# Kernel optimization log

Measured on AMD Instinct MI355X. Metric: run time of the kernel, lower is better.

Reference implementation:

```python
import jax, jax.numpy as jnp
import numpy as np

N, L, H, D = 2, 4096, 12, 64
HD = H * D

def setup_inputs() -> dict:
    key = jax.random.key(0)
    ks = jax.random.split(key, 5)
    s = 1.0 / np.sqrt(HD)  # keep projections well-scaled
    return {
        "x": jax.random.normal(ks[0], (N, L, HD), dtype=jnp.float32),
        "Wq": jax.random.normal(ks[1], (HD, HD), dtype=jnp.float32) * s,
        "bq": jnp.zeros((HD,), dtype=jnp.float32),
        "Wk": jax.random.normal(ks[2], (HD, HD), dtype=jnp.float32) * s,
        "bk": jnp.zeros((HD,), dtype=jnp.float32),
        "Wv": jax.random.normal(ks[3], (HD, HD), dtype=jnp.float32) * s,
        "bv": jnp.zeros((HD,), dtype=jnp.float32),
        "Wo": jax.random.normal(ks[4], (HD, HD), dtype=jnp.float32) * s,
        "bo": jnp.zeros((HD,), dtype=jnp.float32),
        "train": 0,
    }

def reference(x, Wq, bq, Wk, bk, Wv, bv, Wo, bo, train):
    n, l, hd = x.shape
    h, d = H, D
    # QKV projections (hk.Linear: x @ W + b), reshape to (n, l, h, d)
    q = (x @ Wq + bq).reshape(n, l, h, d)
    k = (x @ Wk + bk).reshape(n, l, h, d)
    v = (x @ Wv + bv).reshape(n, l, h, d)
    # scores: (n, q, k, h), scaled by sqrt(key_size)
    qkt = jnp.einsum('nqhd,nkhd->nqkh', q, k) / jnp.sqrt(jnp.float32(d))
    attn = jax.nn.softmax(qkt, axis=2)
    # eval mode: dropout_rate is 0.0, so dropout is identity
    o = jnp.einsum('nqkh,nkhd->nqhd', attn, v).reshape(n, l, hd)
    return o @ Wo + bo
```

## Files before the change

kernel.cpp:

```cpp
#include <hip/hip_runtime.h>

#define NN 2
#define LL 4096
#define HH 12
#define DD 64
#define HD_ 768
#define M_TOT (NN * LL)
#define KVSTRIDE 262144

typedef __bf16 bf16_t;
typedef _Float16 f16_t;
typedef __bf16 bf16x8 __attribute__((ext_vector_type(8)));
typedef __bf16 bf16x4 __attribute__((ext_vector_type(4)));
typedef _Float16 f16x2 __attribute__((ext_vector_type(2)));
typedef _Float16 f16x4 __attribute__((ext_vector_type(4)));
typedef _Float16 f16x8 __attribute__((ext_vector_type(8)));
typedef float floatx4 __attribute__((ext_vector_type(4)));
typedef float floatx16 __attribute__((ext_vector_type(16)));

#define QSCALE 0.1803368801111f

__device__ __forceinline__ void async_load16(const void* g, void* l) {
    __builtin_amdgcn_global_load_lds(
        (const __attribute__((address_space(1))) unsigned int*)(g),
        (__attribute__((address_space(3))) unsigned int*)(l),
        16, 0, 0);
}

__device__ __forceinline__ f16x2 pkrtz(float a, float b) {
    return __builtin_bit_cast(f16x2, __builtin_amdgcn_cvt_pkrtz(a, b));
}

__device__ __forceinline__ f16x4 shflx32(f16x4 v) {
    int2 iv = __builtin_bit_cast(int2, v);
    iv.x = __shfl_xor(iv.x, 32);
    iv.y = __shfl_xor(iv.y, 32);
    return __builtin_bit_cast(f16x4, iv);
}

__global__ void cvt_kernel(const float* __restrict__ src, bf16_t* __restrict__ dst, int n4) {
    int i = blockIdx.x * blockDim.x + threadIdx.x;
    if (i < n4) {
        const float4 v = ((const float4*)src)[i];
        bf16_t* d = dst + (size_t)i * 4;
        d[0] = (bf16_t)v.x; d[1] = (bf16_t)v.y; d[2] = (bf16_t)v.z; d[3] = (bf16_t)v.w;
    }
}

struct WtArgs { const float* W[4]; bf16_t* Wt[4]; };
__global__ void cvt_wt_kernel(WtArgs a) {
    const int z = blockIdx.z;
    int id = blockIdx.x * 256 + threadIdx.x;
    int k = id / HD_;
    int n = id % HD_;
    a.Wt[z][(size_t)n * HD_ + k] = (bf16_t)a.W[z][id];
}

__device__ __forceinline__ void gemm_tile64(
    const bf16_t* __restrict__ A, const bf16_t* __restrict__ Bt,
    bf16_t* As, bf16_t* Bs, int m0, int n0, floatx4 (&acc)[2][2])
{
    const int tid  = threadIdx.x;
    const int lane = tid & 63;
    const int quad = lane >> 4, l16 = lane & 15;
    const int wave = tid >> 6;
    const int wm = wave >> 1, wn = wave & 1;
    const int lrow = tid >> 2;
    const int lcol = (tid & 3) * 16;

    for (int kt = 0; kt < HD_; kt += 64) {
        __syncthreads();
        {
            const bf16_t* ga = A + (size_t)(m0 + lrow) * HD_ + kt + lcol;
            *(bf16x8*)&As[lrow * 72 + lcol]     = *(const bf16x8*)ga;
            *(bf16x8*)&As[lrow * 72 + lcol + 8] = *(const bf16x8*)(ga + 8);
            const bf16_t* gb = Bt + (size_t)(n0 + lrow) * HD_ + kt + lcol;
            *(bf16x8*)&Bs[lrow * 72 + lcol]     = *(const bf16x8*)gb;
            *(bf16x8*)&Bs[lrow * 72 + lcol + 8] = *(const bf16x8*)(gb + 8);
        }
        __syncthreads();
        for (int ks = 0; ks < 2; ++ks) {
            bf16x8 af[2], bfr[2];
            af[0]  = *(const bf16x8*)&As[(wm * 32 + l16) * 72 + ks * 32 + quad * 8];
            af[1]  = *(const bf16x8*)&As[(wm * 32 + 16 + l16) * 72 + ks * 32 + quad * 8];
            bfr[0] = *(const bf16x8*)&Bs[(wn * 32 + l16) * 72 + ks * 32 + quad * 8];
            bfr[1] = *(const bf16x8*)&Bs[(wn * 32 + 16 + l16) * 72 + ks * 32 + quad * 8];
            for (int mi = 0; mi < 2; ++mi)
                for (int ni = 0; ni < 2; ++ni)
                    acc[mi][ni] = __builtin_amdgcn_mfma_f32_16x16x32_bf16(
                        af[mi], bfr[ni], acc[mi][ni], 0, 0, 0);
        }
    }
}

struct QKVArgs {
    const bf16_t* Bt[3];
    const float* bias[3];
    void* out[3];
};
__global__ __launch_bounds__(256) void gemm_qkv_kernel(const bf16_t* __restrict__ A, QKVArgs p)
{
    __shared__ __align__(16) bf16_t As[64 * 72];
    __shared__ __align__(16) bf16_t Bs[64 * 72];
    const int z = blockIdx.z;
    const int m0 = blockIdx.y * 64, n0 = blockIdx.x * 64;

    floatx4 acc[2][2] = {};
    gemm_tile64(A, p.Bt[z], As, Bs, m0, n0, acc);

    const int tid  = threadIdx.x;
    const int lane = tid & 63;
    const int quad = lane >> 4, l16 = lane & 15;
    const int wave = tid >> 6;
    const int wm = wave >> 1, wn = wave & 1;
    const float scale = (z == 0) ? QSCALE : 1.0f;
    const float* bias = p.bias[z];

    for (int ni = 0; ni < 2; ++ni) {
        const int col = n0 + wn * 32 + ni * 16 + l16;
        const float bv = bias[col];
        const int h = col >> 6, d = col & 63;
        for (int mi = 0; mi < 2; ++mi) {
            for (int r = 0; r < 4; ++r) {
                const int row = m0 + wm * 32 + mi * 16 + quad * 4 + r;
                const float val = (acc[mi][ni][r] + bv) * scale;
                const int nn = row >> 12, l = row & 4095;
                const size_t nhb = (size_t)(nn * HH + h) * KVSTRIDE;
                if (z == 0) {
                    ((bf16_t*)p.out[0])[(((size_t)nn * HH + h) * LL + l) * DD + d] = (bf16_t)val;
                } else if (z == 1) {
                    size_t idx = nhb + (size_t)((l >> 5) * 4 + (d >> 4)) * 512
                               + ((l & 31) + 32 * ((d >> 3) & 1)) * 8 + (d & 7);
                    ((bf16_t*)p.out[1])[idx] = (bf16_t)val;
                } else {
                    size_t idx = nhb + (size_t)(((l >> 6) * 2 + (d >> 5)) * 4 + ((l >> 4) & 3)) * 512
                               + ((d & 31) + 32 * ((l >> 3) & 1)) * 8 + (l & 7);
                    ((f16_t*)p.out[2])[idx] = (f16_t)val;
                }
            }
        }
    }
}

__global__ __launch_bounds__(256) void gemm_o_kernel(
    const bf16_t* __restrict__ A, const bf16_t* __restrict__ Bt,
    const float* __restrict__ bias, float* __restrict__ Cout)
{
    __shared__ __align__(16) bf16_t As[64 * 72];
    __shared__ __align__(16) bf16_t Bs[64 * 72];
    const int m0 = blockIdx.y * 64, n0 = blockIdx.x * 64;

    floatx4 acc[2][2] = {};
    gemm_tile64(A, Bt, As, Bs, m0, n0, acc);

    const int tid  = threadIdx.x;
    const int lane = tid & 63;
    const int quad = lane >> 4, l16 = lane & 15;
    const int wave = tid >> 6;
    const int wm = wave >> 1, wn = wave & 1;

    for (int ni = 0; ni < 2; ++ni) {
        const int col = n0 + wn * 32 + ni * 16 + l16;
        const float bv = bias[col];
        for (int mi = 0; mi < 2; ++mi)
            for (int r = 0; r < 4; ++r) {
                const int row = m0 + wm * 32 + mi * 16 + quad * 4 + r;
                Cout[(size_t)row * HD_ + col] = acc[mi][ni][r] + bv;
            }
    }
}

__global__ __launch_bounds__(256) void attn_kernel(
    const bf16_t* __restrict__ qg, const bf16_t* __restrict__ kf,
    const f16_t* __restrict__ vf, bf16_t* __restrict__ og)
{
    __shared__ union {
        struct {
            bf16_t Ks[8 * 512];
            f16_t  Vs[8 * 512];
        } s;
        bf16_t OT[128 * 72];
    } u;

    const int tid = threadIdx.x;
    const int w = tid >> 6, lane = tid & 63;
    const int l32 = lane & 31, hi = lane >> 5;
    const int qt0 = blockIdx.x * 128;
    const int nh = blockIdx.y;
    const int nIdx = nh / HH, hIdx = nh % HH;

    bf16x8 qfrag[4];
    {
        const bf16_t* qp = qg + ((size_t)nh * LL + qt0 + w * 32 + l32) * DD + hi * 8;
        for (int s = 0; s < 4; ++s) qfrag[s] = *(const bf16x8*)(qp + s * 16);
    }

    const bf16_t* ksrc = kf + (size_t)nh * KVSTRIDE + (2 * w) * 512 + lane * 8;
    const f16_t*  vsrc = vf + (size_t)nh * KVSTRIDE + (2 * w) * 512 + lane * 8;
    bf16_t* kdst0 = &u.s.Ks[(2 * w) * 512 + lane * 8];
    bf16_t* kdst1 = &u.s.Ks[(2 * w + 1) * 512 + lane * 8];
    f16_t*  vdst0 = &u.s.Vs[(2 * w) * 512 + lane * 8];
    f16_t*  vdst1 = &u.s.Vs[(2 * w + 1) * 512 + lane * 8];

    floatx16 oacc[2] = {};
    float rs = 0.f;

    for (int t = 0; t < LL / 64; ++t) {
        __syncthreads();
        async_load16(ksrc, kdst0);
        async_load16(ksrc + 512, kdst1);
        async_load16(vsrc, vdst0);
        async_load16(vsrc + 512, vdst1);
        ksrc += 4096; vsrc += 4096;
        __syncthreads();

        for (int kvb = 0; kvb < 2; ++kvb) {
            floatx16 sacc = {};
            for (int s = 0; s < 4; ++s) {
                bf16x8 ak = *(const bf16x8*)&u.s.Ks[(kvb * 4 + s) * 512 + lane * 8];
                sacc = __builtin_amdgcn_mfma_f32_32x32x16_bf16(ak, qfrag[s], sacc, 0, 0, 0);
            }
            for (int sub = 0; sub < 2; ++sub) {
                float p[8];
                for (int i = 0; i < 8; ++i) {
                    p[i] = __builtin_amdgcn_exp2f(sacc[sub * 8 + i]);
                    rs += p[i];
                }
                f16x2 l01 = pkrtz(p[0], p[1]), l23 = pkrtz(p[2], p[3]);
                f16x2 h45 = pkrtz(p[4], p[5]), h67 = pkrtz(p[6], p[7]);
                f16x4 Lo = __builtin_shufflevector(l01, l23, 0, 1, 2, 3);
                f16x4 Hh = __builtin_shufflevector(h45, h67, 0, 1, 2, 3);
                f16x4 swL = shflx32(Lo);
                f16x4 swH = shflx32(Hh);
                f16x4 a03 = hi ? swH : Lo;
                f16x4 a47 = hi ? Hh : swL;
                f16x8 pf = __builtin_shufflevector(a03, a47, 0, 1, 2, 3, 4, 5, 6, 7);
                const int kstep = kvb * 2 + sub;
                for (int db = 0; db < 2; ++db) {
                    f16x8 av = *(const f16x8*)&u.s.Vs[(db * 4 + kstep) * 512 + lane * 8];
                    oacc[db] = __builtin_amdgcn_mfma_f32_32x32x16_f16(av, pf, oacc[db], 0, 0, 0);
                }
            }
        }
    }

    rs += __shfl_xor(rs, 32);
    const float rinv = __builtin_amdgcn_rcpf(rs);

    __syncthreads();
    for (int db = 0; db < 2; ++db)
        for (int g = 0; g < 4; ++g) {
            bf16x4 o4;
            for (int r = 0; r < 4; ++r)
                o4[r] = (bf16_t)(oacc[db][g * 4 + r] * rinv);
            *(bf16x4*)&u.OT[(w * 32 + l32) * 72 + db * 32 + hi * 4 + g * 8] = o4;
        }
    __syncthreads();

    const int q = tid >> 1, hf = tid & 1;
    const bf16_t* src = &u.OT[q * 72 + hf * 32];
    bf16x8 r0 = *(const bf16x8*)(src + 0);
    bf16x8 r1 = *(const bf16x8*)(src + 8);
    bf16x8 r2 = *(const bf16x8*)(src + 16);
    bf16x8 r3 = *(const bf16x8*)(src + 24);
    bf16_t* dst = og + ((size_t)nIdx * LL + qt0 + q) * HD_ + hIdx * 64 + hf * 32;
    *(bf16x8*)(dst + 0)  = r0;
    *(bf16x8*)(dst + 8)  = r1;
    *(bf16x8*)(dst + 16) = r2;
    *(bf16x8*)(dst + 24) = r3;
}

extern "C" void kernel_launch(void* const* d_in, const int* in_sizes, int n_in,
                              void* d_out, int out_size, void* d_ws, size_t ws_size,
                              hipStream_t stream) {
    const float* x  = (const float*)d_in[0];
    const float* Wq = (const float*)d_in[1];
    const float* bq = (const float*)d_in[2];
    const float* Wk = (const float*)d_in[3];
    const float* bk = (const float*)d_in[4];
    const float* Wv = (const float*)d_in[5];
    const float* bv = (const float*)d_in[6];
    const float* Wo = (const float*)d_in[7];
    const float* bo = (const float*)d_in[8];

    char* ws = (char*)d_ws;
    const size_t xbytes = (size_t)M_TOT * HD_ * 2;
    const size_t wbytes = (size_t)HD_ * HD_ * 2;

    bf16_t* xb  = (bf16_t*)ws; ws += xbytes;
    bf16_t* wqt = (bf16_t*)ws; ws += wbytes;
    bf16_t* wkt = (bf16_t*)ws; ws += wbytes;
    bf16_t* wvt = (bf16_t*)ws; ws += wbytes;
    bf16_t* wot = (bf16_t*)ws; ws += wbytes;
    bf16_t* qb  = (bf16_t*)ws; ws += xbytes;
    bf16_t* kfb = (bf16_t*)ws; ws += xbytes;
    f16_t*  vfb = (f16_t*)ws;  ws += xbytes;
    bf16_t* ob  = (bf16_t*)ws; ws += xbytes;

    cvt_kernel<<<(M_TOT * HD_ / 4 + 255) / 256, 256, 0, stream>>>(x, xb, M_TOT * HD_ / 4);

    WtArgs wa;
    wa.W[0] = Wq; wa.W[1] = Wk; wa.W[2] = Wv; wa.W[3] = Wo;
    wa.Wt[0] = wqt; wa.Wt[1] = wkt; wa.Wt[2] = wvt; wa.Wt[3] = wot;
    cvt_wt_kernel<<<dim3(HD_ * HD_ / 256, 1, 4), 256, 0, stream>>>(wa);

    QKVArgs qa;
    qa.Bt[0] = wqt; qa.Bt[1] = wkt; qa.Bt[2] = wvt;
    qa.bias[0] = bq; qa.bias[1] = bk; qa.bias[2] = bv;
    qa.out[0] = qb; qa.out[1] = kfb; qa.out[2] = vfb;
    gemm_qkv_kernel<<<dim3(HD_ / 64, M_TOT / 64, 3), 256, 0, stream>>>(xb, qa);

    attn_kernel<<<dim3(LL / 128, NN * HH), 256, 0, stream>>>(qb, kfb, vfb, ob);

    gemm_o_kernel<<<dim3(HD_ / 64, M_TOT / 64), 256, 0, stream>>>(ob, wot, bo, (float*)d_out);
}
```

Before: 353.3 us.

## Use 128x128 GEMM tiles with direct global-to-LDS async loads

Enlarges the projection GEMM tile to 128x128 with a 4x4 MFMA grid per wave, raising data reuse per LDS load and cutting global traffic. Tile loads now use global_load_lds async copies into an unpadded 64-wide LDS layout instead of register round-trips. It risks LDS bank conflicts from the removed padding, higher register pressure, and fewer blocks for the output GEMM.

```diff
diff --git a/kernel.cpp b/kernel.cpp
--- a/kernel.cpp
+++ b/kernel.cpp
@@ -56,39 +56,38 @@
     a.Wt[z][(size_t)n * HD_ + k] = (bf16_t)a.W[z][id];
 }
 
-__device__ __forceinline__ void gemm_tile64(
+__device__ __forceinline__ void gemm_tile128(
     const bf16_t* __restrict__ A, const bf16_t* __restrict__ Bt,
-    bf16_t* As, bf16_t* Bs, int m0, int n0, floatx4 (&acc)[2][2])
+    bf16_t* As, bf16_t* Bs, int m0, int n0, floatx4 (&acc)[4][4])
 {
     const int tid  = threadIdx.x;
-    const int lane = tid & 63;
+    const int w    = tid >> 6, lane = tid & 63;
     const int quad = lane >> 4, l16 = lane & 15;
-    const int wave = tid >> 6;
-    const int wm = wave >> 1, wn = wave & 1;
-    const int lrow = tid >> 2;
-    const int lcol = (tid & 3) * 16;
+    const int wm = w >> 1, wn = w & 1;
+    const int rsub = lane >> 3;
+    const int csub = (lane & 7) * 8;
+
+    const bf16_t* aBase = A + (size_t)(m0 + w * 32 + rsub) * HD_ + csub;
+    const bf16_t* bBase = Bt + (size_t)(n0 + w * 32 + rsub) * HD_ + csub;
 
     for (int kt = 0; kt < HD_; kt += 64) {
         __syncthreads();
-        {
-            const bf16_t* ga = A + (size_t)(m0 + lrow) * HD_ + kt + lcol;
-            *(bf16x8*)&As[lrow * 72 + lcol]     = *(const bf16x8*)ga;
-            *(bf16x8*)&As[lrow * 72 + lcol + 8] = *(const bf16x8*)(ga + 8);
-            const bf16_t* gb = Bt + (size_t)(n0 + lrow) * HD_ + kt + lcol;
-            *(bf16x8*)&Bs[lrow * 72 + lcol]     = *(const bf16x8*)gb;
-            *(bf16x8*)&Bs[lrow * 72 + lcol + 8] = *(const bf16x8*)(gb + 8);
+        for (int i = 0; i < 4; ++i) {
+            const int ar = w * 32 + i * 8;
+            async_load16(aBase + (size_t)i * 8 * HD_ + kt, As + ar * 64 + lane * 8);
+            async_load16(bBase + (size_t)i * 8 * HD_ + kt, Bs + ar * 64 + lane * 8);
         }
         __syncthreads();
         for (int ks = 0; ks < 2; ++ks) {
-            bf16x8 af[2], bfr[2];
-            af[0]  = *(const bf16x8*)&As[(wm * 32 + l16) * 72 + ks * 32 + quad * 8];
-            af[1]  = *(const bf16x8*)&As[(wm * 32 + 16 + l16) * 72 + ks * 32 + quad * 8];
-            bfr[0] = *(const bf16x8*)&Bs[(wn * 32 + l16) * 72 + ks * 32 + quad * 8];
-            bfr[1] = *(const bf16x8*)&Bs[(wn * 32 + 16 + l16) * 72 + ks * 32 + quad * 8];
-            for (int mi = 0; mi < 2; ++mi)
-                for (int ni = 0; ni < 2; ++ni)
+            bf16x8 af[4], bf[4];
+            for (int mi = 0; mi < 4; ++mi)
+                af[mi] = *(const bf16x8*)&As[(wm * 64 + mi * 16 + l16) * 64 + ks * 32 + quad * 8];
+            for (int ni = 0; ni < 4; ++ni)
+                bf[ni] = *(const bf16x8*)&Bs[(wn * 64 + ni * 16 + l16) * 64 + ks * 32 + quad * 8];
+            for (int mi = 0; mi < 4; ++mi)
+                for (int ni = 0; ni < 4; ++ni)
                     acc[mi][ni] = __builtin_amdgcn_mfma_f32_16x16x32_bf16(
-                        af[mi], bfr[ni], acc[mi][ni], 0, 0, 0);
+                        af[mi], bf[ni], acc[mi][ni], 0, 0, 0);
         }
     }
 }
@@ -100,29 +99,29 @@
 };
 __global__ __launch_bounds__(256) void gemm_qkv_kernel(const bf16_t* __restrict__ A, QKVArgs p)
 {
-    __shared__ __align__(16) bf16_t As[64 * 72];
-    __shared__ __align__(16) bf16_t Bs[64 * 72];
+    __shared__ __align__(16) bf16_t As[128 * 64];
+    __shared__ __align__(16) bf16_t Bs[128 * 64];
     const int z = blockIdx.z;
-    const int m0 = blockIdx.y * 64, n0 = blockIdx.x * 64;
-
-    floatx4 acc[2][2] = {};
-    gemm_tile64(A, p.Bt[z], As, Bs, m0, n0, acc);
+    const int m0 = blockIdx.y * 128, n0 = blockIdx.x * 128;
+
+    floatx4 acc[4][4] = {};
+    gemm_tile128(A, p.Bt[z], As, Bs, m0, n0, acc);
 
     const int tid  = threadIdx.x;
     const int lane = tid & 63;
     const int quad = lane >> 4, l16 = lane & 15;
-    const int wave = tid >> 6;
-    const int wm = wave >> 1, wn = wave & 1;
+    const int w    = tid >> 6;
+    const int wm = w >> 1, wn = w & 1;
     const float scale = (z == 0) ? QSCALE : 1.0f;
     const float* bias = p.bias[z];
 
-    for (int ni = 0; ni < 2; ++ni) {
-        const int col = n0 + wn * 32 + ni * 16 + l16;
+    for (int ni = 0; ni < 4; ++ni) {
+        const int col = n0 + wn * 64 + ni * 16 + l16;
         const float bv = bias[col];
         const int h = col >> 6, d = col & 63;
-        for (int mi = 0; mi < 2; ++mi) {
+        for (int mi = 0; mi < 4; ++mi) {
             for (int r = 0; r < 4; ++r) {
-                const int row = m0 + wm * 32 + mi * 16 + quad * 4 + r;
+                const int row = m0 + wm * 64 + mi * 16 + quad * 4 + r;
                 const float val = (acc[mi][ni][r] + bv) * scale;
                 const int nn = row >> 12, l = row & 4095;
                 const size_t nhb = (size_t)(nn * HH + h) * KVSTRIDE;
@@ -146,25 +145,25 @@
     const bf16_t* __restrict__ A, const bf16_t* __restrict__ Bt,
     const float* __restrict__ bias, float* __restrict__ Cout)
 {
-    __shared__ __align__(16) bf16_t As[64 * 72];
-    __shared__ __align__(16) bf16_t Bs[64 * 72];
-    const int m0 = blockIdx.y * 64, n0 = blockIdx.x * 64;
-
-    floatx4 acc[2][2] = {};
-    gemm_tile64(A, Bt, As, Bs, m0, n0, acc);
+    __shared__ __align__(16) bf16_t As[128 * 64];
+    __shared__ __align__(16) bf16_t Bs[128 * 64];
+    const int m0 = blockIdx.y * 128, n0 = blockIdx.x * 128;
+
+    floatx4 acc[4][4] = {};
+    gemm_tile128(A, Bt, As, Bs, m0, n0, acc);
 
     const int tid  = threadIdx.x;
     const int lane = tid & 63;
     const int quad = lane >> 4, l16 = lane & 15;
-    const int wave = tid >> 6;
-    const int wm = wave >> 1, wn = wave & 1;
-
-    for (int ni = 0; ni < 2; ++ni) {
-        const int col = n0 + wn * 32 + ni * 16 + l16;
+    const int w    = tid >> 6;
+    const int wm = w >> 1, wn = w & 1;
+
+    for (int ni = 0; ni < 4; ++ni) {
+        const int col = n0 + wn * 64 + ni * 16 + l16;
         const float bv = bias[col];
-        for (int mi = 0; mi < 2; ++mi)
+        for (int mi = 0; mi < 4; ++mi)
             for (int r = 0; r < 4; ++r) {
-                const int row = m0 + wm * 32 + mi * 16 + quad * 4 + r;
+                const int row = m0 + wm * 64 + mi * 16 + quad * 4 + r;
                 Cout[(size_t)row * HD_ + col] = acc[mi][ni][r] + bv;
             }
     }
@@ -308,9 +307,9 @@
     qa.Bt[0] = wqt; qa.Bt[1] = wkt; qa.Bt[2] = wvt;
     qa.bias[0] = bq; qa.bias[1] = bk; qa.bias[2] = bv;
     qa.out[0] = qb; qa.out[1] = kfb; qa.out[2] = vfb;
-    gemm_qkv_kernel<<<dim3(HD_ / 64, M_TOT / 64, 3), 256, 0, stream>>>(xb, qa);
+    gemm_qkv_kernel<<<dim3(HD_ / 128, M_TOT / 128, 3), 256, 0, stream>>>(xb, qa);
 
     attn_kernel<<<dim3(LL / 128, NN * HH), 256, 0, stream>>>(qb, kfb, vfb, ob);
 
-    gemm_o_kernel<<<dim3(HD_ / 64, M_TOT / 64), 256, 0, stream>>>(ob, wot, bo, (float*)d_out);
-}
+    gemm_o_kernel<<<dim3(HD_ / 128, M_TOT / 128), 256, 0, stream>>>(ob, wot, bo, (float*)d_out);
+}
```

After: 339.1 us. 1.04x faster.
